# Kernel optimization log

Measured on AMD Instinct MI355X. Metric: run time of the kernel, lower is better.

## Reference

```python
import jax, jax.numpy as jnp
import numpy as np

N_NODES = 100000
N_EDGES = 1600000
NUM_FEATURES = 64
HIDDEN = 64
NUM_CLASSES = 16


def setup_inputs() -> dict:
    key = jax.random.key(0)
    ks = jax.random.split(key, 8)
    x = jax.random.normal(ks[0], (N_NODES, NUM_FEATURES), dtype=jnp.float32)
    edge_index = jax.random.randint(ks[1], (2, N_EDGES), 0, N_NODES, dtype=jnp.int32)
    # Glorot-ish init for weights, zero bias (matches GCNConv / Linear defaults closely enough)
    s1 = 1.0 / np.sqrt(NUM_FEATURES)
    s2 = 1.0 / np.sqrt(HIDDEN)
    W1 = jax.random.uniform(ks[2], (NUM_FEATURES, HIDDEN), jnp.float32, -s1, s1)
    b1 = jnp.zeros((HIDDEN,), jnp.float32)
    W2 = jax.random.uniform(ks[3], (HIDDEN, HIDDEN), jnp.float32, -s2, s2)
    b2 = jnp.zeros((HIDDEN,), jnp.float32)
    W3 = jax.random.uniform(ks[4], (HIDDEN, NUM_CLASSES), jnp.float32, -s2, s2)
    b3 = jax.random.uniform(ks[5], (NUM_CLASSES,), jnp.float32, -s2, s2)
    return {"x": x, "edge_index": edge_index, "W1": W1, "b1": b1,
            "W2": W2, "b2": b2, "W3": W3, "b3": b3}


def _gcn_layer(x, W, b, src, dst, norm, n_nodes):
    # GCNConv: h = X W; out[i] = sum_{(j->i)} norm_ji * h[j]; out += b
    h = x @ W                                   # [N, H] small dense GEMM
    msg = h[src] * norm[:, None]                # [E+N, H] irregular gather
    out = jax.ops.segment_sum(msg, dst, num_segments=n_nodes)  # scatter-add
    return out + b


def reference(x, edge_index, W1, b1, W2, b2, W3, b3):
    n = x.shape[0]
    loop = jnp.arange(n, dtype=edge_index.dtype)
    # add self-loops (PyG GCNConv default add_self_loops=True)
    src = jnp.concatenate([edge_index[0], loop])
    dst = jnp.concatenate([edge_index[1], loop])
    # symmetric normalization D^{-1/2} A_hat D^{-1/2}
    deg = jax.ops.segment_sum(jnp.ones_like(src, dtype=x.dtype), dst, num_segments=n)
    dis = jax.lax.rsqrt(deg)                    # deg >= 1 due to self-loops
    norm = dis[src] * dis[dst]                  # [E+N]

    h = jax.nn.relu(_gcn_layer(x, W1, b1, src, dst, norm, n))
    # F.dropout(training=False) -> identity (module in eval mode)
    h = jax.nn.relu(_gcn_layer(h, W2, b2, src, dst, norm, n))
    z = h @ W3 + b3
    return jax.nn.log_softmax(z, axis=1), h
```

## Files before the change

### kernel.cpp

```cpp
#include <hip/hip_runtime.h>
#include <hip/hip_bf16.h>

typedef __hip_bfloat16 bf16;
typedef unsigned short ushort;

#define NN 100000
#define NE 1600000
#define NBKT 782
#define BCAP 4096
#define EPB 8192
#define NP1 196
#define NMT 6250

typedef __attribute__((ext_vector_type(8))) short s8v;
typedef __attribute__((ext_vector_type(4))) float f4v;

__device__ __forceinline__ float ldf(const void* p, int i, int f32) {
    return f32 ? ((const float*)p)[i] : __bfloat162float(((const bf16*)p)[i]);
}
__device__ __forceinline__ void stf(void* p, int i, int f32, float v) {
    if (f32) ((float*)p)[i] = v;
    else     ((bf16*)p)[i] = __float2bfloat16(v);
}

__device__ __forceinline__ ushort f2b(float f) {
    unsigned u = __builtin_bit_cast(unsigned, f);
    u += 0x7FFF + ((u >> 16) & 1);
    return (ushort)(u >> 16);
}
__device__ __forceinline__ float b2f(ushort h) {
    unsigned u = ((unsigned)h) << 16;
    return __builtin_bit_cast(float, u);
}

__global__ void k_detect(const unsigned* __restrict__ x, int* __restrict__ flag,
                         int* __restrict__ gcur) {
    int gi = blockIdx.x * 256 + threadIdx.x;
    if (gi < 1024) gcur[gi] = 0;
    if (blockIdx.x != 0) return;
    __shared__ int cnt[256];
    int t = threadIdx.x, c = 0;
    for (int i = t; i < 2048; i += 256) {
        unsigned e7 = (x[i] >> 8) & 0x7F;
        c += (e7 >= 60 && e7 <= 66) ? 1 : 0;
    }
    cnt[t] = c;
    __syncthreads();
    for (int s = 128; s > 0; s >>= 1) {
        if (t < s) cnt[t] += cnt[t + s];
        __syncthreads();
    }
    if (t == 0) *flag = (cnt[0] >= 1024) ? 0 : 1;
}

__global__ void k_sentinel(unsigned* out) {
    if (threadIdx.x == 0 && blockIdx.x == 0) out[0] = 0x461C461Cu;
}

__global__ void k_pass1(const int* __restrict__ src, const int* __restrict__ dst,
                        int* __restrict__ gcur, unsigned* __restrict__ bbuf) {
    __shared__ int hist[NBKT];
    __shared__ int base[NBKT];
    int t = threadIdx.x;
    int e0 = blockIdx.x * EPB;
    for (int i = t; i < NBKT; i += 256) hist[i] = 0;
    __syncthreads();
    for (int k = 0; k < EPB; k += 256) {
        int e = e0 + k + t;
        if (e < NE) atomicAdd(&hist[dst[e] >> 7], 1);
    }
    __syncthreads();
    for (int i = t; i < NBKT; i += 256) {
        int c = hist[i];
        base[i] = c ? atomicAdd(&gcur[i], c) : 0;
    }
    __syncthreads();
    for (int i = t; i < NBKT; i += 256) hist[i] = 0;
    __syncthreads();
    for (int k = 0; k < EPB; k += 256) {
        int e = e0 + k + t;
        if (e < NE) {
            int d = dst[e];
            int b = d >> 7;
            int lp = atomicAdd(&hist[b], 1);
            bbuf[b * BCAP + base[b] + lp] = ((unsigned)src[e] << 7) | (unsigned)(d & 127);
        }
    }
}

__global__ void k_scanB(const int* __restrict__ gcur, int* __restrict__ gbase,
                        int* __restrict__ rowptr) {
    __shared__ int s[1024];
    int t = threadIdx.x;
    int v = (t < NBKT) ? gcur[t] : 0;
    s[t] = v;
    __syncthreads();
    for (int d = 1; d < 1024; d <<= 1) {
        int add = (t >= d) ? s[t - d] : 0;
        __syncthreads();
        s[t] += add;
        __syncthreads();
    }
    if (t < NBKT) gbase[t] = s[t] - v;
    if (t == 0) { gbase[NBKT] = NE; rowptr[NN] = NE; }
}

__global__ void k_pass2(const unsigned* __restrict__ bbuf, const int* __restrict__ gbase,
                        int* __restrict__ rowptr, float* __restrict__ dis,
                        int* __restrict__ csr_off) {
    __shared__ unsigned vals[BCAP];
    __shared__ int lout[BCAP];
    __shared__ int fh[128], fx[128], fc[128];
    int b = blockIdx.x, t = threadIdx.x;
    int g0 = gbase[b], cnt = gbase[b + 1] - g0;
    const unsigned* in = bbuf + b * BCAP;
    if (t < 128) fh[t] = 0;
    __syncthreads();
    for (int i = t; i < cnt; i += 256) {
        unsigned v = in[i];
        vals[i] = v;
        atomicAdd(&fh[v & 127], 1);
    }
    __syncthreads();
    if (t < 128) fx[t] = fh[t];
    __syncthreads();
    for (int d = 1; d < 128; d <<= 1) {
        int add = (t >= d && t < 128) ? fx[t - d] : 0;
        __syncthreads();
        if (t < 128) fx[t] += add;
        __syncthreads();
    }
    int n = b * 128 + t;
    if (t < 128) {
        int ex = fx[t] - fh[t];
        fc[t] = ex;
        if (n < NN) {
            rowptr[n] = g0 + ex;
            dis[n] = rsqrtf(1.0f + (float)fh[t]);
        }
    }
    __syncthreads();
    for (int i = t; i < cnt; i += 256) {
        unsigned v = vals[i];
        int p = atomicAdd(&fc[v & 127], 1);
        lout[p] = (int)(v & ~127u);
    }
    __syncthreads();
    for (int i = t; i < cnt; i += 256) csr_off[g0 + i] = lout[i];
}

__global__ void __launch_bounds__(256) k_gemm_mfma(
        const void* __restrict__ A, int aBase, const void* __restrict__ W,
        bf16* __restrict__ C, const float* __restrict__ dis,
        const int* __restrict__ flag) {
    int f32 = *flag;
    int t = threadIdx.x;
    int lane = t & 63;
    int w = t >> 6;
    int m = lane & 15, q = lane >> 4;

    s8v bh[2][4], bl[2][4];
#pragma unroll
    for (int st = 0; st < 2; st++)
#pragma unroll
        for (int nt = 0; nt < 4; nt++)
#pragma unroll
            for (int j = 0; j < 8; j++) {
                int k = st * 32 + q * 8 + j;
                float wv = ldf(W, k * 64 + nt * 16 + m, f32);
                ushort h = f2b(wv);
                bh[st][nt][j] = (short)h;
                bl[st][nt][j] = (short)f2b(wv - b2f(h));
            }

    ushort* Cu = (ushort*)C;
    int gw = blockIdx.x * 4 + w;
    int nw = gridDim.x * 4;
    for (int mt = gw; mt < NMT; mt += nw) {
        int row = mt * 16 + m;
        s8v ah[2], al[2];
        if (f32) {
            const float* ap = (const float*)A + aBase + row * 64 + q * 8;
#pragma unroll
            for (int st = 0; st < 2; st++)
#pragma unroll
                for (int j = 0; j < 8; j++) {
                    float v = ap[st * 32 + j];
                    ushort h = f2b(v);
                    ah[st][j] = (short)h;
                    al[st][j] = (short)f2b(v - b2f(h));
                }
        } else {
            const short* ap = (const short*)A + aBase + row * 64 + q * 8;
            ah[0] = *(const s8v*)(ap);
            ah[1] = *(const s8v*)(ap + 32);
        }
        float dr[4];
#pragma unroll
        for (int r = 0; r < 4; r++) dr[r] = dis[mt * 16 + q * 4 + r];
#pragma unroll
        for (int nt = 0; nt < 4; nt++) {
            f4v acc = {0.f, 0.f, 0.f, 0.f};
#pragma unroll
            for (int st = 0; st < 2; st++)
                acc = __builtin_amdgcn_mfma_f32_16x16x32_bf16(ah[st], bh[st][nt], acc, 0, 0, 0);
            if (f32) {
#pragma unroll
                for (int st = 0; st < 2; st++) {
                    acc = __builtin_amdgcn_mfma_f32_16x16x32_bf16(ah[st], bl[st][nt], acc, 0, 0, 0);
                    acc = __builtin_amdgcn_mfma_f32_16x16x32_bf16(al[st], bh[st][nt], acc, 0, 0, 0);
                }
            }
            int col = nt * 16 + m;
#pragma unroll
            for (int r = 0; r < 4; r++) {
                int rr = mt * 16 + q * 4 + r;
                Cu[rr * 64 + col] = f2b(dr[r] * acc[r]);
            }
        }
    }
}

__global__ void __launch_bounds__(256, 4) k_aggregate(
        const bf16* __restrict__ hs, void* hout, int hoBase,
        const float* __restrict__ dis,
        const int* __restrict__ rowptr,
        const int* __restrict__ csr_off,
        const void* __restrict__ bias,
        const int* __restrict__ flag) {
    int f32 = *flag;
    int pair = blockIdx.x * 4 + (threadIdx.x >> 6);
    int n0 = pair * 2, n1 = n0 + 1;
    int c = threadIdx.x & 63;
    if (n0 >= NN) return;
    const char* hb = (const char*)hs;
    int c2 = c * 2;
    float dn0 = dis[n0], dn1 = dis[n1];
    float self0 = b2f(*(const ushort*)(hb + n0 * 128 + c2));
    float self1 = b2f(*(const ushort*)(hb + n1 * 128 + c2));
    int r0 = rowptr[n0], r1 = rowptr[n0 + 1], r2 = rowptr[n1 + 1];
    int j0 = r0, e0 = r1, j1 = r1, e1 = r2;
    int deg0 = e0 - j0, deg1 = e1 - j1;
    const int F0 = n0 * 128, F1 = n1 * 128;
    float acc0 = self0, acc1 = self1;
    int groups = 0;
    while (j0 < e0 || j1 < e1) {
        int o0[16], o1[16];
#pragma unroll
        for (int k = 0; k < 16; k++) o0[k] = (j0 + k < e0) ? csr_off[j0 + k] : F0;
#pragma unroll
        for (int k = 0; k < 16; k++) o1[k] = (j1 + k < e1) ? csr_off[j1 + k] : F1;
        float v0[16], v1[16];
#pragma unroll
        for (int k = 0; k < 16; k++) v0[k] = b2f(*(const ushort*)(hb + o0[k] + c2));
#pragma unroll
        for (int k = 0; k < 16; k++) v1[k] = b2f(*(const ushort*)(hb + o1[k] + c2));
#pragma unroll
        for (int k = 0; k < 16; k++) { acc0 += v0[k]; acc1 += v1[k]; }
        j0 += 16; j1 += 16; groups++;
    }
    int pad0 = groups * 16 - deg0;
    int pad1 = groups * 16 - deg1;
    acc0 -= (float)pad0 * self0;
    acc1 -= (float)pad1 * self1;
    float bias0 = ldf(bias, c, f32);
    float out0 = fmaxf(dn0 * acc0 + bias0, 0.f);
    float out1 = fmaxf(dn1 * acc1 + bias0, 0.f);
    stf(hout, hoBase + n0 * 64 + c, f32, out0);
    stf(hout, hoBase + n1 * 64 + c, f32, out1);
}

__global__ void k_head(const void* __restrict__ h2, int hBase,
                       const void* __restrict__ W3, const void* __restrict__ b3,
                       void* out, const int* __restrict__ flag) {
    __shared__ float w[64 * 16];
    __shared__ float hrow[16 * 64];
    int f32 = *flag;
    int t = threadIdx.x;
#pragma unroll
    for (int i = 0; i < 4; i++) w[t + i * 256] = ldf(W3, t + i * 256, f32);
    int r0 = blockIdx.x * 16;
#pragma unroll
    for (int i = 0; i < 4; i++) hrow[t + i * 256] = ldf(h2, hBase + r0 * 64 + t + i * 256, f32);
    __syncthreads();
    int lr = t >> 4, c = t & 15;
    float z = ldf(b3, c, f32);
#pragma unroll
    for (int k = 0; k < 64; k++) z += hrow[lr * 64 + k] * w[k * 16 + c];
    float m = z;
#pragma unroll
    for (int off = 8; off >= 1; off >>= 1) m = fmaxf(m, __shfl_xor(m, off, 16));
    float p = expf(z - m);
    float s = p;
#pragma unroll
    for (int off = 8; off >= 1; off >>= 1) s += __shfl_xor(s, off, 16);
    stf(out, (r0 + lr) * 16 + c, f32, z - m - logf(s));
}

extern "C" void kernel_launch(void* const* d_in, const int* in_sizes, int n_in,
                              void* d_out, int out_size, void* d_ws, size_t ws_size,
                              hipStream_t stream) {
    const void* x  = d_in[0];
    const int* ei  = (const int*)d_in[1];
    const void* W1 = d_in[2];
    const void* b1 = d_in[3];
    const void* W2 = d_in[4];
    const void* b2 = d_in[5];
    const void* W3 = d_in[6];
    const void* b3 = d_in[7];

    const size_t NEEDED = (size_t)(1807104 + NBKT * BCAP) * 4;
    if (ws_size < NEEDED) {
        k_sentinel<<<1, 64, 0, stream>>>((unsigned*)d_out);
        return;
    }
    int*      flag    = (int*)d_ws;
    float*    dis     = (float*)d_ws + 256;
    int*      rowptr  = (int*)d_ws + 102656;
    int*      gcur    = (int*)d_ws + 205056;
    int*      gbase   = (int*)d_ws + 206080;
    int*      csr_off = (int*)d_ws + 207104;
    unsigned* bbuf    = (unsigned*)((int*)d_ws + 1807104);
    bf16*     bufA    = (bf16*)bbuf;

    const int* srcp = ei;
    const int* dstp = ei + NE;
    const int HB = NN * 16;

    k_detect<<<4, 256, 0, stream>>>((const unsigned*)x, flag, gcur);

    k_pass1<<<NP1, 256, 0, stream>>>(srcp, dstp, gcur, bbuf);
    k_scanB<<<1, 1024, 0, stream>>>(gcur, gbase, rowptr);
    k_pass2<<<NBKT, 256, 0, stream>>>(bbuf, gbase, rowptr, dis, csr_off);

    k_gemm_mfma<<<512, 256, 0, stream>>>(x, 0, W1, bufA, dis, flag);
    k_aggregate<<<NN / 8, 256, 0, stream>>>(bufA, d_out, HB, dis, rowptr, csr_off, b1, flag);

    k_gemm_mfma<<<512, 256, 0, stream>>>(d_out, HB, W2, bufA, dis, flag);
    k_aggregate<<<NN / 8, 256, 0, stream>>>(bufA, d_out, HB, dis, rowptr, csr_off, b2, flag);

    k_head<<<NN / 16, 256, 0, stream>>>(d_out, HB, W3, b3, d_out, flag);
}
```

Measured before the change: 290.5 us.

## Restructure aggregation: one wavefront per node with 8-byte vector gathers

The aggregation kernel now assigns one wavefront per node instead of two nodes per wavefront with one lane per feature. Each quarter-wave fetches a different neighbor row, and each lane loads 4 bf16 features as a uint2. Partial sums are combined with cross-lane shuffles. Tail edges point at a zero row the GEMM kernel now writes past the last node, which replaces the old pad-and-subtract correction. The aim is wider memory transactions and fewer serialized 2-byte loads per edge, at the cost of shuffle reductions and only a quarter of the lanes doing the final store.

```diff
diff --git a/kernel.cpp b/kernel.cpp
--- a/kernel.cpp
+++ b/kernel.cpp
@@ -31,6 +31,12 @@
 __device__ __forceinline__ float b2f(ushort h) {
     unsigned u = ((unsigned)h) << 16;
     return __builtin_bit_cast(float, u);
+}
+__device__ __forceinline__ float blo(unsigned u) {
+    return __builtin_bit_cast(float, u << 16);
+}
+__device__ __forceinline__ float bhi(unsigned u) {
+    return __builtin_bit_cast(float, u & 0xffff0000u);
 }
 
 __global__ void k_detect(const unsigned* __restrict__ x, int* __restrict__ flag,
@@ -155,6 +161,7 @@
         const int* __restrict__ flag) {
     int f32 = *flag;
     int t = threadIdx.x;
+    if (blockIdx.x == 0 && t < 64) ((ushort*)C)[NN * 64 + t] = 0;
     int lane = t & 63;
     int w = t >> 6;
     int m = lane & 15, q = lane >> 4;
@@ -229,45 +236,72 @@
         const void* __restrict__ bias,
         const int* __restrict__ flag) {
     int f32 = *flag;
-    int pair = blockIdx.x * 4 + (threadIdx.x >> 6);
-    int n0 = pair * 2, n1 = n0 + 1;
-    int c = threadIdx.x & 63;
-    if (n0 >= NN) return;
+    int t = threadIdx.x;
+    int n = blockIdx.x * 4 + (t >> 6);
+    if (n >= NN) return;
+    int l = t & 63;
+    int q = l >> 4;
+    int m = l & 15;
+    int fb = m * 8;
     const char* hb = (const char*)hs;
-    int c2 = c * 2;
-    float dn0 = dis[n0], dn1 = dis[n1];
-    float self0 = b2f(*(const ushort*)(hb + n0 * 128 + c2));
-    float self1 = b2f(*(const ushort*)(hb + n1 * 128 + c2));
-    int r0 = rowptr[n0], r1 = rowptr[n0 + 1], r2 = rowptr[n1 + 1];
-    int j0 = r0, e0 = r1, j1 = r1, e1 = r2;
-    int deg0 = e0 - j0, deg1 = e1 - j1;
-    const int F0 = n0 * 128, F1 = n1 * 128;
-    float acc0 = self0, acc1 = self1;
-    int groups = 0;
-    while (j0 < e0 || j1 < e1) {
-        int o0[16], o1[16];
-#pragma unroll
-        for (int k = 0; k < 16; k++) o0[k] = (j0 + k < e0) ? csr_off[j0 + k] : F0;
-#pragma unroll
-        for (int k = 0; k < 16; k++) o1[k] = (j1 + k < e1) ? csr_off[j1 + k] : F1;
-        float v0[16], v1[16];
-#pragma unroll
-        for (int k = 0; k < 16; k++) v0[k] = b2f(*(const ushort*)(hb + o0[k] + c2));
-#pragma unroll
-        for (int k = 0; k < 16; k++) v1[k] = b2f(*(const ushort*)(hb + o1[k] + c2));
-#pragma unroll
-        for (int k = 0; k < 16; k++) { acc0 += v0[k]; acc1 += v1[k]; }
-        j0 += 16; j1 += 16; groups++;
-    }
-    int pad0 = groups * 16 - deg0;
-    int pad1 = groups * 16 - deg1;
-    acc0 -= (float)pad0 * self0;
-    acc1 -= (float)pad1 * self1;
-    float bias0 = ldf(bias, c, f32);
-    float out0 = fmaxf(dn0 * acc0 + bias0, 0.f);
-    float out1 = fmaxf(dn1 * acc1 + bias0, 0.f);
-    stf(hout, hoBase + n0 * 64 + c, f32, out0);
-    stf(hout, hoBase + n1 * 64 + c, f32, out1);
+    int r0 = rowptr[n], r1 = rowptr[n + 1];
+    float a0 = 0.f, a1 = 0.f, a2 = 0.f, a3 = 0.f;
+    int j = r0;
+    for (; j + 16 <= r1; j += 16) {
+        int o0 = csr_off[j + q];
+        int o1 = csr_off[j + 4 + q];
+        int o2 = csr_off[j + 8 + q];
+        int o3 = csr_off[j + 12 + q];
+        uint2 v0 = *(const uint2*)(hb + o0 + fb);
+        uint2 v1 = *(const uint2*)(hb + o1 + fb);
+        uint2 v2 = *(const uint2*)(hb + o2 + fb);
+        uint2 v3 = *(const uint2*)(hb + o3 + fb);
+        a0 += blo(v0.x); a1 += bhi(v0.x); a2 += blo(v0.y); a3 += bhi(v0.y);
+        a0 += blo(v1.x); a1 += bhi(v1.x); a2 += blo(v1.y); a3 += bhi(v1.y);
+        a0 += blo(v2.x); a1 += bhi(v2.x); a2 += blo(v2.y); a3 += bhi(v2.y);
+        a0 += blo(v3.x); a1 += bhi(v3.x); a2 += blo(v3.y); a3 += bhi(v3.y);
+    }
+    if (j < r1) {
+        const int Z = NN * 128;
+        int i0 = j + q, i1 = j + 4 + q, i2 = j + 8 + q, i3 = j + 12 + q;
+        int o0 = csr_off[i0]; o0 = (i0 < r1) ? o0 : Z;
+        int o1 = csr_off[i1]; o1 = (i1 < r1) ? o1 : Z;
+        int o2 = csr_off[i2]; o2 = (i2 < r1) ? o2 : Z;
+        int o3 = csr_off[i3]; o3 = (i3 < r1) ? o3 : Z;
+        uint2 v0 = *(const uint2*)(hb + o0 + fb);
+        uint2 v1 = *(const uint2*)(hb + o1 + fb);
+        uint2 v2 = *(const uint2*)(hb + o2 + fb);
+        uint2 v3 = *(const uint2*)(hb + o3 + fb);
+        a0 += blo(v0.x); a1 += bhi(v0.x); a2 += blo(v0.y); a3 += bhi(v0.y);
+        a0 += blo(v1.x); a1 += bhi(v1.x); a2 += blo(v1.y); a3 += bhi(v1.y);
+        a0 += blo(v2.x); a1 += bhi(v2.x); a2 += blo(v2.y); a3 += bhi(v2.y);
+        a0 += blo(v3.x); a1 += bhi(v3.x); a2 += blo(v3.y); a3 += bhi(v3.y);
+    }
+    a0 += __shfl_xor(a0, 32); a1 += __shfl_xor(a1, 32);
+    a2 += __shfl_xor(a2, 32); a3 += __shfl_xor(a3, 32);
+    a0 += __shfl_xor(a0, 16); a1 += __shfl_xor(a1, 16);
+    a2 += __shfl_xor(a2, 16); a3 += __shfl_xor(a3, 16);
+    if (q == 0) {
+        uint2 sv = *(const uint2*)(hb + n * 128 + fb);
+        float dn = dis[n];
+        float b0 = ldf(bias, m * 4 + 0, f32);
+        float b1v = ldf(bias, m * 4 + 1, f32);
+        float b2v = ldf(bias, m * 4 + 2, f32);
+        float b3v = ldf(bias, m * 4 + 3, f32);
+        float o0 = fmaxf(dn * (a0 + blo(sv.x)) + b0, 0.f);
+        float o1 = fmaxf(dn * (a1 + bhi(sv.x)) + b1v, 0.f);
+        float o2 = fmaxf(dn * (a2 + blo(sv.y)) + b2v, 0.f);
+        float o3 = fmaxf(dn * (a3 + bhi(sv.y)) + b3v, 0.f);
+        if (f32) {
+            float4 ov = {o0, o1, o2, o3};
+            *(float4*)((float*)hout + hoBase + n * 64 + m * 4) = ov;
+        } else {
+            unsigned w0 = (unsigned)f2b(o0) | ((unsigned)f2b(o1) << 16);
+            unsigned w1 = (unsigned)f2b(o2) | ((unsigned)f2b(o3) << 16);
+            uint2 wv; wv.x = w0; wv.y = w1;
+            *(uint2*)((ushort*)hout + hoBase + n * 64 + m * 4) = wv;
+        }
+    }
 }
 
 __global__ void k_head(const void* __restrict__ h2, int hBase,
@@ -334,10 +368,10 @@
     k_pass2<<<NBKT, 256, 0, stream>>>(bbuf, gbase, rowptr, dis, csr_off);
 
     k_gemm_mfma<<<512, 256, 0, stream>>>(x, 0, W1, bufA, dis, flag);
-    k_aggregate<<<NN / 8, 256, 0, stream>>>(bufA, d_out, HB, dis, rowptr, csr_off, b1, flag);
+    k_aggregate<<<NN / 4, 256, 0, stream>>>(bufA, d_out, HB, dis, rowptr, csr_off, b1, flag);
 
     k_gemm_mfma<<<512, 256, 0, stream>>>(d_out, HB, W2, bufA, dis, flag);
-    k_aggregate<<<NN / 8, 256, 0, stream>>>(bufA, d_out, HB, dis, rowptr, csr_off, b2, flag);
+    k_aggregate<<<NN / 4, 256, 0, stream>>>(bufA, d_out, HB, dis, rowptr, csr_off, b2, flag);
 
     k_head<<<NN / 16, 256, 0, stream>>>(d_out, HB, W3, b3, d_out, flag);
 }
```

Result: faster. 267.2 us (-8.0%).
